# Kernel optimization log

Hardware: AMD Instinct MI355X
Metric: run time of the kernel (lower is better)

Reference implementation:

```python
import jax, jax.numpy as jnp
import numpy as np
import math

B, S, F_IN, D, H = 2048, 100, 158, 512, 8
HD = D // H  # head dim = 64


def _sinusoidal_pe(max_len, d_model):
    pos = np.arange(max_len, dtype=np.float32)[:, None]
    div = np.exp(np.arange(0, d_model, 2, dtype=np.float32) * (-math.log(10000.0) / d_model))
    pe = np.zeros((max_len, d_model), dtype=np.float32)
    pe[:, 0::2] = np.sin(pos * div)
    pe[:, 1::2] = np.cos(pos * div)
    return jnp.asarray(pe)


def setup_inputs() -> dict:
    key = jax.random.key(0)
    ks = jax.random.split(key, 16)
    s = 0.03  # small init scale to keep softmax well-conditioned
    return {
        "src": jax.random.normal(ks[0], (B, S, F_IN), jnp.float32),
        "W_feat": jax.random.normal(ks[1], (D, F_IN), jnp.float32) * s,
        "b_feat": jnp.zeros((D,), jnp.float32),
        "pe": _sinusoidal_pe(100, D),
        "Wq": jax.random.normal(ks[2], (D, D), jnp.float32) * s,
        "bq": jnp.zeros((D,), jnp.float32),
        "Wk": jax.random.normal(ks[3], (D, D), jnp.float32) * s,
        "bk": jnp.zeros((D,), jnp.float32),
        "Wv": jax.random.normal(ks[4], (D, D), jnp.float32) * s,
        "bv": jnp.zeros((D,), jnp.float32),
        "Wo": jax.random.normal(ks[5], (D, D), jnp.float32) * s,
        "bo": jnp.zeros((D,), jnp.float32),
        "ln_w": jnp.ones((D,), jnp.float32),
        "ln_b": jnp.zeros((D,), jnp.float32),
        "W1": jax.random.normal(ks[6], (F_IN, D), jnp.float32) * s,
        "b1": jnp.zeros((F_IN,), jnp.float32),
        "W2": jax.random.normal(ks[7], (D, F_IN), jnp.float32) * s,
        "b2": jnp.zeros((D,), jnp.float32),
        "Wt": jax.random.normal(ks[8], (D, D), jnp.float32) * s,
        "W_out": jax.random.normal(ks[9], (1, D), jnp.float32) * s,
        "b_out": jnp.zeros((1,), jnp.float32),
    }


def _layernorm(x, w, b, eps=1e-5):
    mu = jnp.mean(x, axis=-1, keepdims=True)
    var = jnp.var(x, axis=-1, keepdims=True)
    return (x - mu) * jax.lax.rsqrt(var + eps) * w + b


def reference(src, W_feat, b_feat, pe, Wq, bq, Wk, bk, Wv, bv, Wo, bo,
              ln_w, ln_b, W1, b1, W2, b2, Wt, W_out, b_out):
    # feature projection + sinusoidal PE  (dropout is identity in eval mode)
    x = src @ W_feat.T + b_feat            # [B,S,D]
    x = x + pe[:S]                          # [B,S,D]

    # naive multi-head attention
    def heads(t):  # [B,S,D] -> [B,H,S,HD]
        return t.reshape(B, S, H, HD).transpose(0, 2, 1, 3)
    q = heads(x @ Wq.T + bq)
    k = heads(x @ Wk.T + bk)
    v = heads(x @ Wv.T + bv)
    scores = jnp.einsum('bhqd,bhkd->bhqk', q, k) / jnp.sqrt(jnp.float32(HD))
    probs = jax.nn.softmax(scores, axis=-1)
    attn = jnp.einsum('bhqk,bhkd->bhqd', probs, v)
    attn = attn.transpose(0, 2, 1, 3).reshape(B, S, D)
    attn_out = attn @ Wo.T + bo

    # addnorm #1: x + LayerNorm(x) (note: residual is of the SAME tensor)
    y1 = attn_out + _layernorm(attn_out, ln_w, ln_b)

    # FFN (hidden = 158 per the code's d_ff reuse)
    ffn = jax.nn.relu(y1 @ W1.T + b1) @ W2.T + b2

    # addnorm #2 (same shared AddNormLayer params)
    y2 = ffn + _layernorm(ffn, ln_w, ln_b)

    # temporal attention pooling over time
    h = y2 @ Wt.T                           # [B,S,D]
    lam = jnp.einsum('bsd,bd->bs', h, h[:, -1, :])
    lam = jax.nn.softmax(lam, axis=1)
    pooled = jnp.einsum('bs,bsd->bd', lam, y2)  # [B,D]

    return pooled @ W_out.T + b_out         # [B,1]
```

## Files before the change

kernel.cpp:

```cpp
#include <hip/hip_runtime.h>
#include <math.h>

#define NB 2048
#define NS 100
#define NF 158
#define ND 512
#define NH 8

typedef unsigned short u16;
typedef __attribute__((ext_vector_type(8))) short bf16x8;
typedef __attribute__((ext_vector_type(8))) unsigned short u16x8;
typedef __attribute__((ext_vector_type(4))) float f32x4;

__device__ __forceinline__ u16 f2bf(float f) {
    union { float f; unsigned u; } v; v.f = f;
    unsigned u = v.u;
    return (u16)((u + 0x7fffu + ((u >> 16) & 1u)) >> 16);
}

__device__ __forceinline__ void gload16(const void* g, void* l) {
    __builtin_amdgcn_global_load_lds(
        (const __attribute__((address_space(1))) unsigned*)g,
        (__attribute__((address_space(3))) unsigned*)l, 16, 0, 0);
}

__device__ __forceinline__ bf16x8 load8_cvt(const float* __restrict__ base, int c0) {
    bf16x8 r;
    if (c0 + 8 <= NF) {
        #pragma unroll
        for (int j = 0; j < 8; j += 2) {
            float2 v = *(const float2*)(base + c0 + j);
            r[j] = (short)f2bf(v.x); r[j + 1] = (short)f2bf(v.y);
        }
    } else {
        #pragma unroll
        for (int j = 0; j < 8; ++j)
            r[j] = (c0 + j < NF) ? (short)f2bf(base[c0 + j]) : (short)0;
    }
    return r;
}

__global__ __launch_bounds__(256) void prep_w_kernel(
    const float* __restrict__ Wq, const float* __restrict__ Wk,
    const float* __restrict__ Wv, const float* __restrict__ Wfeat,
    u16* __restrict__ Wf)
{
    int bid = blockIdx.x;
    int sel = bid >> 9;
    int n = bid & 511;
    const float* Wsrc = (sel == 0) ? Wq : (sel == 1) ? Wk : Wv;
    __shared__ float wrow[ND];
    int t = threadIdx.x;
    wrow[t] = Wsrc[(size_t)n * ND + t];
    wrow[t + 256] = Wsrc[(size_t)n * ND + t + 256];
    __syncthreads();
    if (t < 160) {
        float acc = 0.f;
        if (t < NF)
            for (int d = 0; d < ND; ++d)
                acc += wrow[d] * Wfeat[(size_t)d * NF + t];
        int h = n >> 6, ni = (n >> 4) & 3, l16 = n & 15;
        int ks = t >> 5, quad = (t >> 3) & 3, j = t & 7;
        size_t idx = (((((size_t)sel * 8 + h) * 4 + ni) * 5 + ks) * 64
                      + (quad << 4) + l16) * 8 + j;
        Wf[idx] = f2bf(acc);
    }
}

__global__ __launch_bounds__(256) void prep_c_kernel(
    const float* __restrict__ Wq, const float* __restrict__ Wk, const float* __restrict__ Wv,
    const float* __restrict__ bq, const float* __restrict__ bk, const float* __restrict__ bv,
    const float* __restrict__ bfeat, const float* __restrict__ pe,
    float* __restrict__ Cqkv)
{
    int bid = blockIdx.x;
    int sel = bid / 100;
    int s = bid - sel * 100;
    const float* Wsrc = (sel == 0) ? Wq : (sel == 1) ? Wk : Wv;
    const float* bsrc = (sel == 0) ? bq : (sel == 1) ? bk : bv;
    __shared__ float xv[ND];
    int t = threadIdx.x;
    xv[t] = bfeat[t] + pe[(size_t)s * ND + t];
    xv[t + 256] = bfeat[t + 256] + pe[(size_t)s * ND + t + 256];
    __syncthreads();
    #pragma unroll
    for (int rr = 0; rr < 2; ++rr) {
        int r = t + (rr << 8);
        const float* wr = Wsrc + (size_t)r * ND;
        float acc = bsrc[r];
        for (int d = 0; d < ND; d += 4) {
            float4 w4 = *(const float4*)(wr + d);
            acc += w4.x * xv[d] + w4.y * xv[d+1] + w4.z * xv[d+2] + w4.w * xv[d+3];
        }
        Cqkv[(size_t)s * 1536 + (sel << 9) + r] = acc;
    }
}

__global__ __launch_bounds__(256) void pad_cast_kernel(
    const float* __restrict__ src, u16* __restrict__ dst,
    int R, int C, int Cp, int total)
{
    int idx = blockIdx.x * 256 + threadIdx.x;
    if (idx >= total) return;
    int r = idx / Cp, c = idx - r * Cp;
    float v = (r < R && c < C) ? src[(size_t)r * C + c] : 0.f;
    dst[idx] = f2bf(v);
}

__global__ __launch_bounds__(256) void pad_b1_kernel(
    const float* __restrict__ b1, float* __restrict__ b1p)
{
    int t = threadIdx.x;
    b1p[t] = (t < NF) ? b1[t] : 0.f;
}

#define ALDQ 72
#define ALDP 136

__global__ __launch_bounds__(256) void qkv_attn_kernel(
    const float* __restrict__ src, const u16* __restrict__ Wf,
    const float* __restrict__ tab, u16* __restrict__ O)
{
    __shared__ short UN[128 * ALDP];
    __shared__ short Ks[112 * ALDQ];
    __shared__ short Vt[64 * ALDP];

    int t = threadIdx.x;
    int lane = t & 63, wave = t >> 6;
    int quad = lane >> 4, l16 = lane & 15;
    int rows0 = wave << 5;
    int b = blockIdx.x;
    const float* xb = src + (size_t)b * NS * NF;
    const size_t rowbase = (size_t)b * NS;
    f32x4 z = {0.f, 0.f, 0.f, 0.f};

    for (int l = t; l < 12 * ALDQ; l += 256)
        Ks[(100 + l / ALDQ) * ALDQ + (l % ALDQ)] = 0;
    for (int l = t; l < 64 * 28; l += 256) {
        int d = l / 28, s = 100 + (l - d * 28);
        Vt[d * ALDP + s] = 0;
    }

    bf16x8 AF[2][5];
    #pragma unroll
    for (int mt = 0; mt < 2; ++mt) {
        int row = rows0 + (mt << 4) + l16;
        const float* xr = xb + (size_t)row * NF;
        #pragma unroll
        for (int ks = 0; ks < 5; ++ks) {
            if (row < NS) AF[mt][ks] = load8_cvt(xr, (ks << 5) + (quad << 3));
            else { bf16x8 zz = {0,0,0,0,0,0,0,0}; AF[mt][ks] = zz; }
        }
    }

    for (int h = 0; h < NH; ++h) {
        #pragma unroll
        for (int sel = 0; sel < 3; ++sel) {
            f32x4 acc[2][4];
            #pragma unroll
            for (int mt = 0; mt < 2; ++mt)
                #pragma unroll
                for (int ni = 0; ni < 4; ++ni) acc[mt][ni] = z;
            #pragma unroll
            for (int ks = 0; ks < 5; ++ks) {
                bf16x8 wfr[4];
                #pragma unroll
                for (int ni = 0; ni < 4; ++ni)
                    wfr[ni] = *(const bf16x8*)(Wf +
                        (((((size_t)sel * 8 + h) * 4 + ni) * 5 + ks) * 64 + lane) * 8);
                #pragma unroll
                for (int mt = 0; mt < 2; ++mt)
                    #pragma unroll
                    for (int ni = 0; ni < 4; ++ni)
                        acc[mt][ni] = __builtin_amdgcn_mfma_f32_16x16x32_bf16(
                            AF[mt][ks], wfr[ni], acc[mt][ni], 0, 0, 0);
            }
            #pragma unroll
            for (int mt = 0; mt < 2; ++mt) {
                int rbase = rows0 + (mt << 4) + (quad << 2);
                #pragma unroll
                for (int r = 0; r < 4; ++r) {
                    int row_s = rbase + r;
                    bool real = row_s < NS;
                    const float* trow = tab + (size_t)(real ? row_s : 0) * 1536
                                        + (sel << 9) + (h << 6);
                    #pragma unroll
                    for (int ni = 0; ni < 4; ++ni) {
                        int nloc = (ni << 4) + l16;
                        float v = acc[mt][ni][r] + (real ? trow[nloc] : 0.f);
                        u16 bv = f2bf(v);
                        if (sel == 0) UN[row_s * ALDP + nloc] = (short)bv;
                        else if (sel == 1) { if (real) Ks[row_s * ALDQ + nloc] = (short)bv; }
                        else               { if (real) Vt[nloc * ALDP + row_s] = (short)bv; }
                    }
                }
            }
        }
        __syncthreads();

        f32x4 sc[2][7];
        #pragma unroll
        for (int mi = 0; mi < 2; ++mi)
            #pragma unroll
            for (int ni = 0; ni < 7; ++ni) sc[mi][ni] = z;
        #pragma unroll
        for (int ks = 0; ks < 2; ++ks) {
            bf16x8 aq[2], bk[7];
            #pragma unroll
            for (int mi = 0; mi < 2; ++mi)
                aq[mi] = *(const bf16x8*)&UN[(rows0 + (mi << 4) + l16) * ALDP + (ks << 5) + (quad << 3)];
            #pragma unroll
            for (int ni = 0; ni < 7; ++ni)
                bk[ni] = *(const bf16x8*)&Ks[((ni << 4) + l16) * ALDQ + (ks << 5) + (quad << 3)];
            #pragma unroll
            for (int mi = 0; mi < 2; ++mi)
                #pragma unroll
                for (int ni = 0; ni < 7; ++ni)
                    sc[mi][ni] = __builtin_amdgcn_mfma_f32_16x16x32_bf16(aq[mi], bk[ni], sc[mi][ni], 0, 0, 0);
        }
        __syncthreads();

        #pragma unroll
        for (int mi = 0; mi < 2; ++mi) {
            #pragma unroll
            for (int r = 0; r < 4; ++r) {
                if (l16 >= 4) sc[mi][6][r] = -3.0e38f;
                float mx = sc[mi][0][r];
                #pragma unroll
                for (int ni = 1; ni < 7; ++ni) mx = fmaxf(mx, sc[mi][ni][r]);
                #pragma unroll
                for (int off = 1; off < 16; off <<= 1) mx = fmaxf(mx, __shfl_xor(mx, off));
                float sum = 0.f;
                #pragma unroll
                for (int ni = 0; ni < 7; ++ni) {
                    float e = expf((sc[mi][ni][r] - mx) * 0.125f);
                    sc[mi][ni][r] = e; sum += e;
                }
                #pragma unroll
                for (int off = 1; off < 16; off <<= 1) sum += __shfl_xor(sum, off);
                float inv = 1.f / sum;
                int row = rows0 + (mi << 4) + (quad << 2) + r;
                #pragma unroll
                for (int ni = 0; ni < 7; ++ni)
                    UN[row * ALDP + (ni << 4) + l16] = (short)f2bf(sc[mi][ni][r] * inv);
                UN[row * ALDP + 112 + l16] = 0;
            }
        }
        __syncthreads();

        f32x4 oa[2][4];
        #pragma unroll
        for (int mi = 0; mi < 2; ++mi)
            #pragma unroll
            for (int ni = 0; ni < 4; ++ni) oa[mi][ni] = z;
        #pragma unroll
        for (int ks = 0; ks < 4; ++ks) {
            bf16x8 ap[2], bv[4];
            #pragma unroll
            for (int mi = 0; mi < 2; ++mi)
                ap[mi] = *(const bf16x8*)&UN[(rows0 + (mi << 4) + l16) * ALDP + (ks << 5) + (quad << 3)];
            #pragma unroll
            for (int ni = 0; ni < 4; ++ni)
                bv[ni] = *(const bf16x8*)&Vt[((ni << 4) + l16) * ALDP + (ks << 5) + (quad << 3)];
            #pragma unroll
            for (int mi = 0; mi < 2; ++mi)
                #pragma unroll
                for (int ni = 0; ni < 4; ++ni)
                    oa[mi][ni] = __builtin_amdgcn_mfma_f32_16x16x32_bf16(ap[mi], bv[ni], oa[mi][ni], 0, 0, 0);
        }
        #pragma unroll
        for (int mi = 0; mi < 2; ++mi) {
            #pragma unroll
            for (int r = 0; r < 4; ++r) {
                int row = rows0 + (mi << 4) + (quad << 2) + r;
                if (row < NS) {
                    u16* orow = O + (rowbase + row) * 512 + (h << 6);
                    #pragma unroll
                    for (int ni = 0; ni < 4; ++ni)
                        orow[(ni << 4) + l16] = f2bf(oa[mi][ni][r]);
                }
            }
        }
        __syncthreads();
    }
}

template<int OUTMODE, bool RELU>
__global__ __launch_bounds__(256) void gemm_bf16(
    const u16* __restrict__ A, const u16* __restrict__ W,
    const float* __restrict__ bias, void* __restrict__ Cv, int K, int ldc)
{
    __shared__ short As[128 * 32];
    __shared__ short Bs[128 * 32];
    int t = threadIdx.x;
    int lane = t & 63, wave = t >> 6;
    int quad = lane >> 4, l16 = lane & 15;
    int wr = wave >> 1, wc = wave & 1;
    int m0 = blockIdx.y << 7, n0 = blockIdx.x << 7;

    f32x4 acc[4][4];
    f32x4 z = {0.f, 0.f, 0.f, 0.f};
    #pragma unroll
    for (int mi = 0; mi < 4; ++mi)
        #pragma unroll
        for (int ni = 0; ni < 4; ++ni) acc[mi][ni] = z;

    int rowA = t >> 2;
    int cch = (t & 3) << 3;
    const u16* aSrc0 = A + (size_t)(m0 + rowA) * K + cch;
    const u16* aSrc1 = A + (size_t)(m0 + rowA + 64) * K + cch;
    const u16* bSrc0 = W + (size_t)(n0 + rowA) * K + cch;
    const u16* bSrc1 = W + (size_t)(n0 + rowA + 64) * K + cch;
    short* aDst0 = As + t * 8;
    short* aDst1 = As + (t + 256) * 8;
    short* bDst0 = Bs + t * 8;
    short* bDst1 = Bs + (t + 256) * 8;

    int nk = K >> 5;
    for (int kc = 0; kc < nk; ++kc) {
        if (kc) __syncthreads();
        gload16(aSrc0, aDst0);
        gload16(aSrc1, aDst1);
        gload16(bSrc0, bDst0);
        gload16(bSrc1, bDst1);
        aSrc0 += 32; aSrc1 += 32; bSrc0 += 32; bSrc1 += 32;
        __syncthreads();

        bf16x8 af[4], bw[4];
        #pragma unroll
        for (int mi = 0; mi < 4; ++mi)
            af[mi] = *(const bf16x8*)(As + ((size_t)((wr << 6) + (mi << 4) + l16) * 32 + (quad << 3)));
        #pragma unroll
        for (int ni = 0; ni < 4; ++ni)
            bw[ni] = *(const bf16x8*)(Bs + ((size_t)((wc << 6) + (ni << 4) + l16) * 32 + (quad << 3)));
        #pragma unroll
        for (int mi = 0; mi < 4; ++mi)
            #pragma unroll
            for (int ni = 0; ni < 4; ++ni)
                acc[mi][ni] = __builtin_amdgcn_mfma_f32_16x16x32_bf16(af[mi], bw[ni], acc[mi][ni], 0, 0, 0);
    }

    #pragma unroll
    for (int mi = 0; mi < 4; ++mi) {
        #pragma unroll
        for (int r = 0; r < 4; ++r) {
            int row = m0 + (wr << 6) + (mi << 4) + (quad << 2) + r;
            #pragma unroll
            for (int ni = 0; ni < 4; ++ni) {
                int col = n0 + (wc << 6) + (ni << 4) + l16;
                float v = acc[mi][ni][r];
                if (bias) v += bias[col];
                if (RELU) v = fmaxf(v, 0.f);
                if (OUTMODE == 0)
                    ((float*)Cv)[(size_t)row * ldc + col] = v;
                else
                    ((u16*)Cv)[(size_t)row * ldc + col] = f2bf(v);
            }
        }
    }
}

template<int OUTMODE>
__global__ __launch_bounds__(512, 2) void gemm_ln(
    const u16* __restrict__ A, const u16* __restrict__ W,
    const float* __restrict__ bias, const float* __restrict__ lnw,
    const float* __restrict__ lnb, void* __restrict__ outv, int K)
{
    __shared__ short As[64 * 32];
    __shared__ short Bs[512 * 32];
    __shared__ float red_s[64][9];
    __shared__ float red_q[64][9];
    __shared__ float mrow[64], rrow[64];

    int t = threadIdx.x;
    int lane = t & 63, wave = t >> 6;
    int quad = lane >> 4, l16 = lane & 15;
    int m0 = blockIdx.x << 6;

    f32x4 acc[4][4];
    f32x4 z = {0.f, 0.f, 0.f, 0.f};
    #pragma unroll
    for (int mi = 0; mi < 4; ++mi)
        #pragma unroll
        for (int ni = 0; ni < 4; ++ni) acc[mi][ni] = z;

    int koff = (t & 3) << 3;
    const u16* aSrc = A + (size_t)(m0 + (t >> 2)) * K + koff;
    const u16* bSrc0 = W + (size_t)(t >> 2) * K + koff;
    const u16* bSrc1 = W + (size_t)((t >> 2) + 128) * K + koff;
    const u16* bSrc2 = W + (size_t)((t >> 2) + 256) * K + koff;
    const u16* bSrc3 = W + (size_t)((t >> 2) + 384) * K + koff;
    short* aDst = As + t * 8;
    short* bDst0 = Bs + t * 8;
    short* bDst1 = Bs + (t + 512) * 8;
    short* bDst2 = Bs + (t + 1024) * 8;
    short* bDst3 = Bs + (t + 1536) * 8;

    int nk = K >> 5;
    for (int kc = 0; kc < nk; ++kc) {
        if (kc) __syncthreads();
        if (t < 256) gload16(aSrc, aDst);
        gload16(bSrc0, bDst0);
        gload16(bSrc1, bDst1);
        gload16(bSrc2, bDst2);
        gload16(bSrc3, bDst3);
        aSrc += 32; bSrc0 += 32; bSrc1 += 32; bSrc2 += 32; bSrc3 += 32;
        __syncthreads();

        bf16x8 af[4], bw[4];
        #pragma unroll
        for (int mi = 0; mi < 4; ++mi)
            af[mi] = *(const bf16x8*)(As + ((mi << 4) + l16) * 32 + (quad << 3));
        #pragma unroll
        for (int ni = 0; ni < 4; ++ni)
            bw[ni] = *(const bf16x8*)(Bs + ((wave << 6) + (ni << 4) + l16) * 32 + (quad << 3));
        #pragma unroll
        for (int mi = 0; mi < 4; ++mi)
            #pragma unroll
            for (int ni = 0; ni < 4; ++ni)
                acc[mi][ni] = __builtin_amdgcn_mfma_f32_16x16x32_bf16(af[mi], bw[ni], acc[mi][ni], 0, 0, 0);
    }

    float lwv[4], lbv[4];
    #pragma unroll
    for (int ni = 0; ni < 4; ++ni) {
        int col = (wave << 6) + (ni << 4) + l16;
        float bv = bias[col];
        lwv[ni] = lnw[col];
        lbv[ni] = lnb[col];
        #pragma unroll
        for (int mi = 0; mi < 4; ++mi)
            #pragma unroll
            for (int r = 0; r < 4; ++r) acc[mi][ni][r] += bv;
    }
    #pragma unroll
    for (int mi = 0; mi < 4; ++mi) {
        #pragma unroll
        for (int r = 0; r < 4; ++r) {
            float s = acc[mi][0][r] + acc[mi][1][r] + acc[mi][2][r] + acc[mi][3][r];
            float q = acc[mi][0][r]*acc[mi][0][r] + acc[mi][1][r]*acc[mi][1][r]
                    + acc[mi][2][r]*acc[mi][2][r] + acc[mi][3][r]*acc[mi][3][r];
            #pragma unroll
            for (int off = 1; off < 16; off <<= 1) {
                s += __shfl_xor(s, off);
                q += __shfl_xor(q, off);
            }
            if (l16 == 0) {
                int row = (mi << 4) + (quad << 2) + r;
                red_s[row][wave] = s;
                red_q[row][wave] = q;
            }
        }
    }
    __syncthreads();
    if (t < 64) {
        float s = 0.f, q = 0.f;
        #pragma unroll
        for (int w8 = 0; w8 < 8; ++w8) { s += red_s[t][w8]; q += red_q[t][w8]; }
        float mean = s * (1.f / 512.f);
        float var = q * (1.f / 512.f) - mean * mean;
        mrow[t] = mean;
        rrow[t] = rsqrtf(var + 1e-5f);
    }
    __syncthreads();
    #pragma unroll
    for (int mi = 0; mi < 4; ++mi) {
        #pragma unroll
        for (int r = 0; r < 4; ++r) {
            int lrow = (mi << 4) + (quad << 2) + r;
            float mean = mrow[lrow], rstd = rrow[lrow];
            size_t grow = (size_t)(m0 + lrow) * 512;
            #pragma unroll
            for (int ni = 0; ni < 4; ++ni) {
                int col = (wave << 6) + (ni << 4) + l16;
                float v = acc[mi][ni][r];
                float y = v + (v - mean) * rstd * lwv[ni] + lbv[ni];
                if (OUTMODE == 0) ((float*)outv)[grow + col] = y;
                else ((u16*)outv)[grow + col] = f2bf(y);
            }
        }
    }
}

__global__ __launch_bounds__(256) void u_stage1_kernel(
    const float* __restrict__ Y2, const float* __restrict__ Wt,
    float* __restrict__ T1)
{
    __shared__ float yl[16][512];
    int t = threadIdx.x;
    int r0 = blockIdx.x << 6;
    int bg = blockIdx.y << 4;
    for (int l = t; l < 2048; l += 256) {
        int bb = l >> 7, seg = (l & 127) << 2;
        *(float4*)&yl[bb][seg] =
            *(const float4*)&Y2[((size_t)(bg + bb) * NS + 99) * ND + seg];
    }
    __syncthreads();
    int r = r0 + (t & 63);
    int b0 = t >> 6;
    const float* wr = Wt + (size_t)r * ND;
    float acc[4] = {0.f, 0.f, 0.f, 0.f};
    for (int d = 0; d < ND; d += 4) {
        float4 w4 = *(const float4*)(wr + d);
        #pragma unroll
        for (int bb = 0; bb < 4; ++bb) {
            int bl = (b0 << 2) + bb;
            acc[bb] += w4.x * yl[bl][d] + w4.y * yl[bl][d+1]
                     + w4.z * yl[bl][d+2] + w4.w * yl[bl][d+3];
        }
    }
    #pragma unroll
    for (int bb = 0; bb < 4; ++bb)
        T1[(size_t)(bg + (b0 << 2) + bb) * ND + r] = acc[bb];
}

__global__ __launch_bounds__(256) void u_stage2_kernel(
    const float* __restrict__ T1, const float* __restrict__ Wt,
    float* __restrict__ U)
{
    __shared__ float t1s[16][512];
    int t = threadIdx.x;
    int c0 = blockIdx.x << 6;
    int bg = blockIdx.y << 4;
    for (int l = t; l < 2048; l += 256) {
        int bb = l >> 7, seg = (l & 127) << 2;
        *(float4*)&t1s[bb][seg] = *(const float4*)&T1[(size_t)(bg + bb) * ND + seg];
    }
    __syncthreads();
    int c = c0 + (t & 63);
    int b0 = t >> 6;
    float acc[4] = {0.f, 0.f, 0.f, 0.f};
    for (int r = 0; r < ND; ++r) {
        float w = Wt[(size_t)r * ND + c];
        #pragma unroll
        for (int bb = 0; bb < 4; ++bb)
            acc[bb] += w * t1s[(b0 << 2) + bb][r];
    }
    #pragma unroll
    for (int bb = 0; bb < 4; ++bb)
        U[(size_t)(bg + (b0 << 2) + bb) * ND + c] = acc[bb];
}

__global__ __launch_bounds__(256) void pool_kernel(
    const float* __restrict__ Y2, const float* __restrict__ U,
    const float* __restrict__ Wout, const float* __restrict__ bout,
    float* __restrict__ out)
{
    __shared__ float u[ND];
    __shared__ float lam[128];
    __shared__ float red[4];
    int t = threadIdx.x;
    int b = blockIdx.x;
    const float* y2b = Y2 + (size_t)b * NS * ND;
    u[t] = U[(size_t)b * ND + t];
    u[t + 256] = U[(size_t)b * ND + t + 256];
    __syncthreads();
    int wid = t >> 6, lane = t & 63;
    int c0 = lane << 2;
    for (int s = wid; s < NS; s += 4) {
        const float* yr = y2b + (size_t)s * ND;
        float4 p0 = *(const float4*)(yr + c0);
        float4 p1 = *(const float4*)(yr + 256 + c0);
        float a = p0.x*u[c0] + p0.y*u[c0+1] + p0.z*u[c0+2] + p0.w*u[c0+3]
                + p1.x*u[256+c0] + p1.y*u[256+c0+1] + p1.z*u[256+c0+2] + p1.w*u[256+c0+3];
        #pragma unroll
        for (int off = 32; off > 0; off >>= 1) a += __shfl_xor(a, off);
        if (lane == 0) lam[s] = a;
    }
    __syncthreads();
    if (t < 64) {
        float l0 = lam[t];
        float l1 = (t + 64 < NS) ? lam[t + 64] : -3.0e38f;
        float mx = fmaxf(l0, l1);
        #pragma unroll
        for (int off = 32; off > 0; off >>= 1) mx = fmaxf(mx, __shfl_xor(mx, off));
        float e0 = expf(l0 - mx);
        float e1 = (t + 64 < NS) ? expf(l1 - mx) : 0.f;
        float ssum = e0 + e1;
        #pragma unroll
        for (int off = 32; off > 0; off >>= 1) ssum += __shfl_xor(ssum, off);
        float inv = 1.f / ssum;
        lam[t] = e0 * inv;
        if (t + 64 < NS) lam[t + 64] = e1 * inv;
    }
    __syncthreads();
    float p0 = 0.f, p1 = 0.f;
    for (int s = 0; s < NS; ++s) {
        float lm = lam[s];
        const float* yr = y2b + (size_t)s * ND;
        p0 += lm * yr[t];
        p1 += lm * yr[t + 256];
    }
    float vd = p0 * Wout[t] + p1 * Wout[t + 256];
    #pragma unroll
    for (int off = 32; off > 0; off >>= 1) vd += __shfl_xor(vd, off);
    if (lane == 0) red[wid] = vd;
    __syncthreads();
    if (t == 0) out[b] = red[0] + red[1] + red[2] + red[3] + bout[0];
}

static size_t ws_need(int CBc) {
    size_t cm = (size_t)CBc * NS;
    size_t b = 0;
    b += cm * 512 * 2;
    b += cm * 512 * 2;
    b += cm * 256 * 2;
    b += cm * 512 * 4;
    b += (size_t)CBc * 512 * 4 * 2;
    b += 1536 * 160 * 2;
    b += 512 * 512 * 2 + 256 * 512 * 2 + 512 * 256 * 2;
    b += 100 * 1536 * 4 + 256 * 4;
    b += 64 * 1024;
    return b;
}

extern "C" void kernel_launch(void* const* d_in, const int* in_sizes, int n_in,
                              void* d_out, int out_size, void* d_ws, size_t ws_size,
                              hipStream_t stream)
{
    const float* src   = (const float*)d_in[0];
    const float* Wfeat = (const float*)d_in[1];
    const float* bfeat = (const float*)d_in[2];
    const float* pe    = (const float*)d_in[3];
    const float* Wq    = (const float*)d_in[4];
    const float* bq    = (const float*)d_in[5];
    const float* Wk    = (const float*)d_in[6];
    const float* bk    = (const float*)d_in[7];
    const float* Wv    = (const float*)d_in[8];
    const float* bv    = (const float*)d_in[9];
    const float* Wo    = (const float*)d_in[10];
    const float* bo    = (const float*)d_in[11];
    const float* lnw   = (const float*)d_in[12];
    const float* lnb   = (const float*)d_in[13];
    const float* W1    = (const float*)d_in[14];
    const float* b1    = (const float*)d_in[15];
    const float* W2    = (const float*)d_in[16];
    const float* b2    = (const float*)d_in[17];
    const float* Wt    = (const float*)d_in[18];
    const float* Wout  = (const float*)d_in[19];
    const float* bout  = (const float*)d_in[20];
    float* out = (float*)d_out;

    int CBc = (ws_size >= ws_need(1024)) ? 1024
            : (ws_size >= ws_need(512))  ? 512
            : (ws_size >= ws_need(256))  ? 256 : 128;
    int NCH = NB / CBc;
    size_t CMc = (size_t)CBc * NS;

    char* p = (char*)d_ws;
    auto alloc = [&](size_t bytes) { char* r = p; p += (bytes + 255) & ~(size_t)255; return r; };
    u16*   AO16  = (u16*)  alloc(CMc * 512 * 2);
    u16*   Y116  = (u16*)  alloc(CMc * 512 * 2);
    u16*   ACT16 = (u16*)  alloc(CMc * 256 * 2);
    float* Y2    = (float*)alloc(CMc * 512 * 4);
    float* T1    = (float*)alloc((size_t)CBc * 512 * 4);
    float* U     = (float*)alloc((size_t)CBc * 512 * 4);
    u16*   Wf    = (u16*)  alloc(1536 * 160 * 2);
    u16*   Wo16  = (u16*)  alloc(512 * 512 * 2);
    u16*   W116  = (u16*)  alloc(256 * 512 * 2);
    u16*   W216  = (u16*)  alloc(512 * 256 * 2);
    float* Cqkv  = (float*)alloc(100 * 1536 * 4);
    float* b1p   = (float*)alloc(256 * 4);

    prep_w_kernel<<<1536, 256, 0, stream>>>(Wq, Wk, Wv, Wfeat, Wf);
    prep_c_kernel<<<300, 256, 0, stream>>>(Wq, Wk, Wv, bq, bk, bv, bfeat, pe, Cqkv);
    pad_cast_kernel<<<(512 * 512) / 256, 256, 0, stream>>>(Wo, Wo16, 512, 512, 512, 512 * 512);
    pad_cast_kernel<<<(256 * 512) / 256, 256, 0, stream>>>(W1, W116, NF, 512, 512, 256 * 512);
    pad_cast_kernel<<<(512 * 256) / 256, 256, 0, stream>>>(W2, W216, 512, NF, 256, 512 * 256);
    pad_b1_kernel<<<1, 256, 0, stream>>>(b1, b1p);

    dim3 g256(2, CMc / 128);
    dim3 gU(8, CBc / 16);
    int gLN = CMc / 64;

    for (int c = 0; c < NCH; ++c) {
        const float* srcC = src + (size_t)c * CMc * NF;
        float* outC = out + (size_t)c * CBc;

        qkv_attn_kernel<<<CBc, 256, 0, stream>>>(srcC, Wf, Cqkv, AO16);
        gemm_ln<1><<<gLN, 512, 0, stream>>>(AO16, Wo16, bo, lnw, lnb, Y116, 512);
        gemm_bf16<1, true><<<g256, 256, 0, stream>>>(Y116, W116, b1p, ACT16, 512, 256);
        gemm_ln<0><<<gLN, 512, 0, stream>>>(ACT16, W216, b2, lnw, lnb, Y2, 256);
        u_stage1_kernel<<<gU, 256, 0, stream>>>(Y2, Wt, T1);
        u_stage2_kernel<<<gU, 256, 0, stream>>>(T1, Wt, U);
        pool_kernel<<<CBc, 256, 0, stream>>>(Y2, U, Wout, bout, outC);
    }

    (void)in_sizes; (void)n_in; (void)out_size; (void)ws_size;
}
```

Before: 1.833 ms.

## Split attention kernel across 8 waves and vectorize bias-table loads

The fused QKV+attention kernel now launches 512 threads per batch element, so each wave handles 16 query rows instead of 32. This halves the per-wave accumulator and fragment register footprint and adds parallelism within each block. The precomputed bias/PE table is re-laid out per (sel, head, row) so each lane fetches its four column values with one float4 load instead of four scalar loads. The trade-off is that every wave now re-loads the same Wf fragments from global memory for half the MFMA work, and the larger blocks may limit how many fit per CU because of LDS.

```diff
diff --git a/kernel.cpp b/kernel.cpp
--- a/kernel.cpp
+++ b/kernel.cpp
@@ -71,7 +71,7 @@
     const float* __restrict__ Wq, const float* __restrict__ Wk, const float* __restrict__ Wv,
     const float* __restrict__ bq, const float* __restrict__ bk, const float* __restrict__ bv,
     const float* __restrict__ bfeat, const float* __restrict__ pe,
-    float* __restrict__ Cqkv)
+    float* __restrict__ T4)
 {
     int bid = blockIdx.x;
     int sel = bid / 100;
@@ -92,7 +92,8 @@
             float4 w4 = *(const float4*)(wr + d);
             acc += w4.x * xv[d] + w4.y * xv[d+1] + w4.z * xv[d+2] + w4.w * xv[d+3];
         }
-        Cqkv[(size_t)s * 1536 + (sel << 9) + r] = acc;
+        int h = r >> 6, ni = (r >> 4) & 3, l16 = r & 15;
+        T4[(((size_t)(sel * 8 + h)) * 100 + s) * 64 + (l16 << 2) + ni] = acc;
     }
 }
 
@@ -117,9 +118,9 @@
 #define ALDQ 72
 #define ALDP 136
 
-__global__ __launch_bounds__(256) void qkv_attn_kernel(
+__global__ __launch_bounds__(512, 4) void qkv_attn_kernel(
     const float* __restrict__ src, const u16* __restrict__ Wf,
-    const float* __restrict__ tab, u16* __restrict__ O)
+    const float* __restrict__ T4, u16* __restrict__ O)
 {
     __shared__ short UN[128 * ALDP];
     __shared__ short Ks[112 * ALDQ];
@@ -128,39 +129,36 @@
     int t = threadIdx.x;
     int lane = t & 63, wave = t >> 6;
     int quad = lane >> 4, l16 = lane & 15;
-    int rows0 = wave << 5;
+    int rows0 = wave << 4;
     int b = blockIdx.x;
     const float* xb = src + (size_t)b * NS * NF;
     const size_t rowbase = (size_t)b * NS;
     f32x4 z = {0.f, 0.f, 0.f, 0.f};
 
-    for (int l = t; l < 12 * ALDQ; l += 256)
+    for (int l = t; l < 12 * ALDQ; l += 512)
         Ks[(100 + l / ALDQ) * ALDQ + (l % ALDQ)] = 0;
-    for (int l = t; l < 64 * 28; l += 256) {
+    for (int l = t; l < 64 * 28; l += 512) {
         int d = l / 28, s = 100 + (l - d * 28);
         Vt[d * ALDP + s] = 0;
     }
 
-    bf16x8 AF[2][5];
-    #pragma unroll
-    for (int mt = 0; mt < 2; ++mt) {
-        int row = rows0 + (mt << 4) + l16;
-        const float* xr = xb + (size_t)row * NF;
+    int arow = rows0 + l16;
+    bf16x8 AF[5];
+    {
+        const float* xr = xb + (size_t)arow * NF;
         #pragma unroll
         for (int ks = 0; ks < 5; ++ks) {
-            if (row < NS) AF[mt][ks] = load8_cvt(xr, (ks << 5) + (quad << 3));
-            else { bf16x8 zz = {0,0,0,0,0,0,0,0}; AF[mt][ks] = zz; }
+            if (arow < NS) AF[ks] = load8_cvt(xr, (ks << 5) + (quad << 3));
+            else { bf16x8 zz = {0,0,0,0,0,0,0,0}; AF[ks] = zz; }
         }
     }
 
     for (int h = 0; h < NH; ++h) {
         #pragma unroll
         for (int sel = 0; sel < 3; ++sel) {
-            f32x4 acc[2][4];
-            #pragma unroll
-            for (int mt = 0; mt < 2; ++mt)
-                #pragma unroll
-                for (int ni = 0; ni < 4; ++ni) acc[mt][ni] = z;
+            f32x4 acc[4];
+            #pragma unroll
+            for (int ni = 0; ni < 4; ++ni) acc[ni] = z;
             #pragma unroll
             for (int ks = 0; ks < 5; ++ks) {
                 bf16x8 wfr[4];
@@ -169,116 +167,95 @@
                     wfr[ni] = *(const bf16x8*)(Wf +
                         (((((size_t)sel * 8 + h) * 4 + ni) * 5 + ks) * 64 + lane) * 8);
                 #pragma unroll
-                for (int mt = 0; mt < 2; ++mt)
-                    #pragma unroll
-                    for (int ni = 0; ni < 4; ++ni)
-                        acc[mt][ni] = __builtin_amdgcn_mfma_f32_16x16x32_bf16(
-                            AF[mt][ks], wfr[ni], acc[mt][ni], 0, 0, 0);
-            }
-            #pragma unroll
-            for (int mt = 0; mt < 2; ++mt) {
-                int rbase = rows0 + (mt << 4) + (quad << 2);
+                for (int ni = 0; ni < 4; ++ni)
+                    acc[ni] = __builtin_amdgcn_mfma_f32_16x16x32_bf16(
+                        AF[ks], wfr[ni], acc[ni], 0, 0, 0);
+            }
+            #pragma unroll
+            for (int r = 0; r < 4; ++r) {
+                int row_s = rows0 + (quad << 2) + r;
+                bool real = row_s < NS;
+                float4 tv = make_float4(0.f, 0.f, 0.f, 0.f);
+                if (real)
+                    tv = *(const float4*)(T4 +
+                        (((size_t)(sel * 8 + h)) * 100 + row_s) * 64 + (l16 << 2));
+                float tvs[4] = {tv.x, tv.y, tv.z, tv.w};
                 #pragma unroll
-                for (int r = 0; r < 4; ++r) {
-                    int row_s = rbase + r;
-                    bool real = row_s < NS;
-                    const float* trow = tab + (size_t)(real ? row_s : 0) * 1536
-                                        + (sel << 9) + (h << 6);
-                    #pragma unroll
-                    for (int ni = 0; ni < 4; ++ni) {
-                        int nloc = (ni << 4) + l16;
-                        float v = acc[mt][ni][r] + (real ? trow[nloc] : 0.f);
-                        u16 bv = f2bf(v);
-                        if (sel == 0) UN[row_s * ALDP + nloc] = (short)bv;
-                        else if (sel == 1) { if (real) Ks[row_s * ALDQ + nloc] = (short)bv; }
-                        else               { if (real) Vt[nloc * ALDP + row_s] = (short)bv; }
-                    }
+                for (int ni = 0; ni < 4; ++ni) {
+                    int nloc = (ni << 4) + l16;
+                    float v = acc[ni][r] + tvs[ni];
+                    u16 bv = f2bf(v);
+                    if (sel == 0) UN[row_s * ALDP + nloc] = (short)bv;
+                    else if (sel == 1) { if (real) Ks[row_s * ALDQ + nloc] = (short)bv; }
+                    else               { if (real) Vt[nloc * ALDP + row_s] = (short)bv; }
                 }
             }
         }
         __syncthreads();
 
-        f32x4 sc[2][7];
-        #pragma unroll
-        for (int mi = 0; mi < 2; ++mi)
-            #pragma unroll
-            for (int ni = 0; ni < 7; ++ni) sc[mi][ni] = z;
+        f32x4 sc[7];
+        #pragma unroll
+        for (int ni = 0; ni < 7; ++ni) sc[ni] = z;
         #pragma unroll
         for (int ks = 0; ks < 2; ++ks) {
-            bf16x8 aq[2], bk[7];
-            #pragma unroll
-            for (int mi = 0; mi < 2; ++mi)
-                aq[mi] = *(const bf16x8*)&UN[(rows0 + (mi << 4) + l16) * ALDP + (ks << 5) + (quad << 3)];
+            bf16x8 aq = *(const bf16x8*)&UN[(rows0 + l16) * ALDP + (ks << 5) + (quad << 3)];
+            bf16x8 bk[7];
             #pragma unroll
             for (int ni = 0; ni < 7; ++ni)
                 bk[ni] = *(const bf16x8*)&Ks[((ni << 4) + l16) * ALDQ + (ks << 5) + (quad << 3)];
             #pragma unroll
-            for (int mi = 0; mi < 2; ++mi)
-                #pragma unroll
-                for (int ni = 0; ni < 7; ++ni)
-                    sc[mi][ni] = __builtin_amdgcn_mfma_f32_16x16x32_bf16(aq[mi], bk[ni], sc[mi][ni], 0, 0, 0);
+            for (int ni = 0; ni < 7; ++ni)
+                sc[ni] = __builtin_amdgcn_mfma_f32_16x16x32_bf16(aq, bk[ni], sc[ni], 0, 0, 0);
         }
         __syncthreads();
 
         #pragma unroll
-        for (int mi = 0; mi < 2; ++mi) {
-            #pragma unroll
-            for (int r = 0; r < 4; ++r) {
-                if (l16 >= 4) sc[mi][6][r] = -3.0e38f;
-                float mx = sc[mi][0][r];
-                #pragma unroll
-                for (int ni = 1; ni < 7; ++ni) mx = fmaxf(mx, sc[mi][ni][r]);
-                #pragma unroll
-                for (int off = 1; off < 16; off <<= 1) mx = fmaxf(mx, __shfl_xor(mx, off));
-                float sum = 0.f;
-                #pragma unroll
-                for (int ni = 0; ni < 7; ++ni) {
-                    float e = expf((sc[mi][ni][r] - mx) * 0.125f);
-                    sc[mi][ni][r] = e; sum += e;
-                }
-                #pragma unroll
-                for (int off = 1; off < 16; off <<= 1) sum += __shfl_xor(sum, off);
-                float inv = 1.f / sum;
-                int row = rows0 + (mi << 4) + (quad << 2) + r;
-                #pragma unroll
-                for (int ni = 0; ni < 7; ++ni)
-                    UN[row * ALDP + (ni << 4) + l16] = (short)f2bf(sc[mi][ni][r] * inv);
-                UN[row * ALDP + 112 + l16] = 0;
-            }
+        for (int r = 0; r < 4; ++r) {
+            if (l16 >= 4) sc[6][r] = -3.0e38f;
+            float mx = sc[0][r];
+            #pragma unroll
+            for (int ni = 1; ni < 7; ++ni) mx = fmaxf(mx, sc[ni][r]);
+            #pragma unroll
+            for (int off = 1; off < 16; off <<= 1) mx = fmaxf(mx, __shfl_xor(mx, off));
+            float sum = 0.f;
+            #pragma unroll
+            for (int ni = 0; ni < 7; ++ni) {
+                float e = expf((sc[ni][r] - mx) * 0.125f);
+                sc[ni][r] = e; sum += e;
+            }
+            #pragma unroll
+            for (int off = 1; off < 16; off <<= 1) sum += __shfl_xor(sum, off);
+            float inv = 1.f / sum;
+            int row = rows0 + (quad << 2) + r;
+            #pragma unroll
+            for (int ni = 0; ni < 7; ++ni)
+                UN[row * ALDP + (ni << 4) + l16] = (short)f2bf(sc[ni][r] * inv);
+            UN[row * ALDP + 112 + l16] = 0;
         }
         __syncthreads();
 
-        f32x4 oa[2][4];
-        #pragma unroll
-        for (int mi = 0; mi < 2; ++mi)
-            #pragma unroll
-            for (int ni = 0; ni < 4; ++ni) oa[mi][ni] = z;
+        f32x4 oa[4];
+        #pragma unroll
+        for (int ni = 0; ni < 4; ++ni) oa[ni] = z;
         #pragma unroll
         for (int ks = 0; ks < 4; ++ks) {
-            bf16x8 ap[2], bv[4];
-            #pragma unroll
-            for (int mi = 0; mi < 2; ++mi)
-                ap[mi] = *(const bf16x8*)&UN[(rows0 + (mi << 4) + l16) * ALDP + (ks << 5) + (quad << 3)];
+            bf16x8 ap = *(const bf16x8*)&UN[(rows0 + l16) * ALDP + (ks << 5) + (quad << 3)];
+            bf16x8 bv[4];
             #pragma unroll
             for (int ni = 0; ni < 4; ++ni)
                 bv[ni] = *(const bf16x8*)&Vt[((ni << 4) + l16) * ALDP + (ks << 5) + (quad << 3)];
             #pragma unroll
-            for (int mi = 0; mi < 2; ++mi)
+            for (int ni = 0; ni < 4; ++ni)
+                oa[ni] = __builtin_amdgcn_mfma_f32_16x16x32_bf16(ap, bv[ni], oa[ni], 0, 0, 0);
+        }
+        #pragma unroll
+        for (int r = 0; r < 4; ++r) {
+            int row = rows0 + (quad << 2) + r;
+            if (row < NS) {
+                u16* orow = O + (rowbase + row) * 512 + (h << 6);
                 #pragma unroll
                 for (int ni = 0; ni < 4; ++ni)
-                    oa[mi][ni] = __builtin_amdgcn_mfma_f32_16x16x32_bf16(ap[mi], bv[ni], oa[mi][ni], 0, 0, 0);
-        }
-        #pragma unroll
-        for (int mi = 0; mi < 2; ++mi) {
-            #pragma unroll
-            for (int r = 0; r < 4; ++r) {
-                int row = rows0 + (mi << 4) + (quad << 2) + r;
-                if (row < NS) {
-                    u16* orow = O + (rowbase + row) * 512 + (h << 6);
-                    #pragma unroll
-                    for (int ni = 0; ni < 4; ++ni)
-                        orow[(ni << 4) + l16] = f2bf(oa[mi][ni][r]);
-                }
+                    orow[(ni << 4) + l16] = f2bf(oa[ni][r]);
             }
         }
         __syncthreads();
@@ -609,7 +586,8 @@
     b += (size_t)CBc * 512 * 4 * 2;
     b += 1536 * 160 * 2;
     b += 512 * 512 * 2 + 256 * 512 * 2 + 512 * 256 * 2;
-    b += 100 * 1536 * 4 + 256 * 4;
+    b += 3 * 8 * 100 * 64 * 4;
+    b += 256 * 4;
     b += 64 * 1024;
     return b;
 }
@@ -659,11 +637,11 @@
     u16*   Wo16  = (u16*)  alloc(512 * 512 * 2);
     u16*   W116  = (u16*)  alloc(256 * 512 * 2);
     u16*   W216  = (u16*)  alloc(512 * 256 * 2);
-    float* Cqkv  = (float*)alloc(100 * 1536 * 4);
+    float* T4    = (float*)alloc(3 * 8 * 100 * 64 * 4);
     float* b1p   = (float*)alloc(256 * 4);
 
     prep_w_kernel<<<1536, 256, 0, stream>>>(Wq, Wk, Wv, Wfeat, Wf);
-    prep_c_kernel<<<300, 256, 0, stream>>>(Wq, Wk, Wv, bq, bk, bv, bfeat, pe, Cqkv);
+    prep_c_kernel<<<300, 256, 0, stream>>>(Wq, Wk, Wv, bq, bk, bv, bfeat, pe, T4);
     pad_cast_kernel<<<(512 * 512) / 256, 256, 0, stream>>>(Wo, Wo16, 512, 512, 512, 512 * 512);
     pad_cast_kernel<<<(256 * 512) / 256, 256, 0, stream>>>(W1, W116, NF, 512, 512, 256 * 512);
     pad_cast_kernel<<<(512 * 256) / 256, 256, 0, stream>>>(W2, W216, 512, NF, 256, 512 * 256);
@@ -677,7 +655,7 @@
         const float* srcC = src + (size_t)c * CMc * NF;
         float* outC = out + (size_t)c * CBc;
 
-        qkv_attn_kernel<<<CBc, 256, 0, stream>>>(srcC, Wf, Cqkv, AO16);
+        qkv_attn_kernel<<<CBc, 512, 0, stream>>>(srcC, Wf, T4, AO16);
         gemm_ln<1><<<gLN, 512, 0, stream>>>(AO16, Wo16, bo, lnw, lnb, Y116, 512);
         gemm_bf16<1, true><<<g256, 256, 0, stream>>>(Y116, W116, b1p, ACT16, 512, 256);
         gemm_ln<0><<<gLN, 512, 0, stream>>>(ACT16, W216, b2, lnw, lnb, Y2, 256);
```

Measured after the change: 1.552 ms. -15.3%, faster.
